# Optimization experiments

Hardware: AMD Instinct MI355X
Metric: run time of the kernel (lower is better)

## Reference

```python
import jax, jax.numpy as jnp
import numpy as np

N_HEADS, D_MODEL, DK, DV = 16, 1024, 64, 64
B, S = 4, 2048


def setup_inputs() -> dict:
    key = jax.random.key(0)
    ks = jax.random.split(key, 7)
    scale = 1.0 / np.sqrt(D_MODEL)
    return {
        "Q": jax.random.normal(ks[0], (B, S, D_MODEL), dtype=jnp.float32),
        "K": jax.random.normal(ks[1], (B, S, D_MODEL), dtype=jnp.float32),
        "V": jax.random.normal(ks[2], (B, S, D_MODEL), dtype=jnp.float32),
        # Linear weights stored as [in, out] so y = x @ W (equivalent to torch x @ W.T)
        "w_q": jax.random.normal(ks[3], (D_MODEL, N_HEADS * DK), dtype=jnp.float32) * scale,
        "w_k": jax.random.normal(ks[4], (D_MODEL, N_HEADS * DK), dtype=jnp.float32) * scale,
        "w_v": jax.random.normal(ks[5], (D_MODEL, N_HEADS * DV), dtype=jnp.float32) * scale,
        "w_o": jax.random.normal(ks[6], (N_HEADS * DV, D_MODEL), dtype=jnp.float32) * scale,
    }


def reference(Q, K, V, w_q, w_k, w_v, w_o):
    b, s, _ = Q.shape
    # projections -> [B, H, S, d]
    q = (Q @ w_q).reshape(b, s, N_HEADS, DK).transpose(0, 2, 1, 3)
    k = (K @ w_k).reshape(b, s, N_HEADS, DK).transpose(0, 2, 1, 3)
    v = (V @ w_v).reshape(b, s, N_HEADS, DV).transpose(0, 2, 1, 3)
    # scaled dot-product attention, full [B,H,S,S] scores (matches source)
    scores = jnp.einsum("bhqd,bhkd->bhqk", q, k) / jnp.sqrt(jnp.float32(DK))
    attn = jax.nn.softmax(scores, axis=-1)
    x = jnp.einsum("bhqk,bhkd->bhqd", attn, v)
    x = x.transpose(0, 2, 1, 3).reshape(b, s, N_HEADS * DV)
    return x @ w_o
```

## Files before the change

kernel.cpp:

```cpp
#include <hip/hip_runtime.h>
#include <stdint.h>

#define B_   4
#define S_   2048
#define H_   16
#define D_   64
#define DM_  1024
#define NTOK (B_ * S_)

typedef __attribute__((ext_vector_type(8))) short short8;
typedef __attribute__((ext_vector_type(4))) float floatx4;

__device__ inline unsigned short f2bf(float f) {
  unsigned int u = __float_as_uint(f);
  u += 0x7FFFu + ((u >> 16) & 1u);
  return (unsigned short)(u >> 16);
}

__device__ inline floatx4 mfma_bf16(short8 a, short8 b, floatx4 c) {
  return __builtin_amdgcn_mfma_f32_16x16x32_bf16(a, b, c, 0, 0, 0);
}

__device__ inline unsigned int pack_bf2(float lo, float hi) {
  return __builtin_amdgcn_perm(__float_as_uint(hi), __float_as_uint(lo), 0x07060302u);
}

__device__ inline void gload_lds16(const unsigned short* g, unsigned short* l) {
  __builtin_amdgcn_global_load_lds(
      (const __attribute__((address_space(1))) unsigned int*)g,
      (__attribute__((address_space(3))) unsigned int*)l, 16, 0, 0);
}

__global__ __launch_bounds__(256) void cast_bf16_kernel(const float* __restrict__ in,
                                                        unsigned short* __restrict__ out,
                                                        int n4) {
  int i = blockIdx.x * 256 + threadIdx.x;
  if (i < n4) {
    float4 v = ((const float4*)in)[i];
    ushort4 o;
    o.x = f2bf(v.x); o.y = f2bf(v.y); o.z = f2bf(v.z); o.w = f2bf(v.w);
    ((ushort4*)out)[i] = o;
  }
}

__global__ __launch_bounds__(256) void wt_kernel(const float* __restrict__ w0,
                                                 const float* __restrict__ w1,
                                                 const float* __restrict__ w2,
                                                 const float* __restrict__ w3,
                                                 unsigned short* __restrict__ o0,
                                                 unsigned short* __restrict__ o1,
                                                 unsigned short* __restrict__ o2,
                                                 unsigned short* __restrict__ o3) {
  __shared__ unsigned short T[64 * 68];
  const float* w = blockIdx.z == 0 ? w0 : blockIdx.z == 1 ? w1 : blockIdx.z == 2 ? w2 : w3;
  unsigned short* o = blockIdx.z == 0 ? o0 : blockIdx.z == 1 ? o1 : blockIdx.z == 2 ? o2 : o3;
  const int tid = threadIdx.x;
  const int R0 = blockIdx.y * 64;
  const int C0 = blockIdx.x * 64;
  for (int it = 0; it < 16; it++) {
    int lr = it * 4 + (tid >> 6), lc = tid & 63;
    T[lc * 68 + lr] = f2bf(w[(size_t)(R0 + lr) * 1024 + C0 + lc]);
  }
  __syncthreads();
  for (int it = 0; it < 2; it++) {
    int orow = it * 32 + (tid >> 3), oc = (tid & 7) * 8;
    union { ushort4 h[2]; short8 v8; } u;
    u.h[0] = *(const ushort4*)(T + orow * 68 + oc);
    u.h[1] = *(const ushort4*)(T + orow * 68 + oc + 4);
    *(short8*)(o + (size_t)(C0 + orow) * 1024 + R0 + oc) = u.v8;
  }
}

template <int MODE>
__global__ __launch_bounds__(256) void gemm_bt_kernel(const unsigned short* __restrict__ A,
                                                      const unsigned short* __restrict__ BT,
                                                      void* __restrict__ Cout,
                                                      float scale) {
  constexpr int K = 1024;
  __shared__ unsigned short As[128 * 32];
  __shared__ unsigned short Bs[128 * 32];

  const int tid  = threadIdx.x;
  const int wave = tid >> 6, lane = tid & 63;
  const int quad = lane >> 4, l16 = lane & 15;
  const int wm = wave >> 1, wn = wave & 1;
  const int m0 = blockIdx.y * 128, n0 = blockIdx.x * 128;

  floatx4 acc[4][4] = {};

  for (int k0 = 0; k0 < K; k0 += 32) {
    for (int p = 0; p < 2; p++) {
      int i = p * 256 + wave * 64 + lane;
      int row = i >> 2, c = i & 3;
      gload_lds16(A  + (size_t)(m0 + row) * K + k0 + c * 8,
                  As + (size_t)(p * 256 + wave * 64) * 8);
      gload_lds16(BT + (size_t)(n0 + row) * K + k0 + c * 8,
                  Bs + (size_t)(p * 256 + wave * 64) * 8);
    }
    __syncthreads();

    short8 af[4], bfr[4];
    for (int f = 0; f < 4; f++) {
      af[f]  = *(const short8*)(As + (wm * 64 + f * 16 + l16) * 32 + quad * 8);
      bfr[f] = *(const short8*)(Bs + (wn * 64 + f * 16 + l16) * 32 + quad * 8);
    }
    for (int fm = 0; fm < 4; fm++)
      for (int fn = 0; fn < 4; fn++)
        acc[fm][fn] = mfma_bf16(af[fm], bfr[fn], acc[fm][fn]);
    __syncthreads();
  }

  for (int fm = 0; fm < 4; fm++)
    for (int fn = 0; fn < 4; fn++)
      for (int r = 0; r < 4; r++) {
        int gm = m0 + wm * 64 + fm * 16 + quad * 4 + r;
        int gn = n0 + wn * 64 + fn * 16 + l16;
        float val = acc[fm][fn][r] * scale;
        if (MODE == 0) {
          int b = gm >> 11, s = gm & 2047;
          int h = gn >> 6,  d = gn & 63;
          ((unsigned short*)Cout)[((size_t)((b * H_ + h) * S_ + s) << 6) + d] = f2bf(val);
        } else if (MODE == 1) {
          ((float*)Cout)[((size_t)gm << 10) + gn] = val;
        } else {
          int b = gm >> 11, s = gm & 2047;
          int h = gn >> 6,  d = gn & 63;
          int p = ((s & 63) >> 4) + (s & 15) * 4;
          ((unsigned short*)Cout)[(((size_t)(b * H_ + h) * 64 + d) << 11) + (s & ~63) + p] = f2bf(val);
        }
      }
}

__global__ __launch_bounds__(256, 2) void attn_kernel(const unsigned short* __restrict__ q,
                                                      const unsigned short* __restrict__ k,
                                                      const unsigned short* __restrict__ vT,
                                                      unsigned short* __restrict__ X) {
  __shared__ unsigned short Ks[64 * 64];
  __shared__ unsigned short Vt[64 * 64];
  __shared__ unsigned short Ps[4][16 * 72];

  const int tid  = threadIdx.x;
  const int wave = tid >> 6, lane = tid & 63;
  const int quad = lane >> 4, l16 = lane & 15;
  const int bh = blockIdx.y;
  const int q0 = blockIdx.x * 256;

  const unsigned short* qh = q  + (size_t)bh * S_ * 64;
  const unsigned short* kh = k  + (size_t)bh * S_ * 64;
  const unsigned short* vh = vT + (size_t)bh * 64 * S_;

  short8 qf[4][2];
  for (int qt = 0; qt < 4; qt++) {
    int row = q0 + wave * 64 + qt * 16 + l16;
    for (int kk = 0; kk < 2; kk++)
      qf[qt][kk] = *(const short8*)(qh + (size_t)row * 64 + kk * 32 + quad * 8);
  }

  short8 onesb = {};
  if (l16 == 0)
    for (int e = 0; e < 8; e++) onesb[e] = (short)0x3F80;

  floatx4 O[4][4] = {};
  floatx4 lacc[4] = {};

  for (int j0 = 0; j0 < S_; j0 += 64) {
    __syncthreads();

    for (int p = 0; p < 2; p++) {
      int i = p * 256 + tid;
      int r = i >> 3;
      int gc = (i & 7) ^ (r & 7);
      gload_lds16(kh + (size_t)(j0 + r) * 64 + gc * 8,
                  Ks + (size_t)(p * 256 + wave * 64) * 8);
      gload_lds16(vh + (size_t)r * S_ + j0 + gc * 8,
                  Vt + (size_t)(p * 256 + wave * 64) * 8);
    }
    __syncthreads();

    short8 kf[4][2];
    for (int jf = 0; jf < 4; jf++)
      for (int kk = 0; kk < 2; kk++) {
        int sl = (kk * 4 + quad) ^ (l16 & 7);
        kf[jf][kk] = *(const short8*)(Ks + (jf * 16 + l16) * 64 + sl * 8);
      }
    short8 vf[4][2];
    for (int df = 0; df < 4; df++)
      for (int jk = 0; jk < 2; jk++) {
        int sl = (jk * 4 + quad) ^ (l16 & 7);
        vf[df][jk] = *(const short8*)(Vt + (df * 16 + l16) * 64 + sl * 8);
      }

    unsigned short* pw = Ps[wave];
    for (int qt = 0; qt < 4; qt++) {
      floatx4 s[4] = {};
      for (int jf = 0; jf < 4; jf++) {
        s[jf] = mfma_bf16(qf[qt][0], kf[jf][0], s[jf]);
        s[jf] = mfma_bf16(qf[qt][1], kf[jf][1], s[jf]);
      }
      for (int r = 0; r < 4; r++) {
        float e0 = exp2f(s[0][r]), e1 = exp2f(s[1][r]);
        float e2 = exp2f(s[2][r]), e3 = exp2f(s[3][r]);
        uint2 pk;
        pk.x = pack_bf2(e0, e1);
        pk.y = pack_bf2(e2, e3);
        *(uint2*)(pw + (quad * 4 + r) * 72 + l16 * 4) = pk;
      }
      short8 pa0 = *(const short8*)(pw + l16 * 72 + quad * 8);
      short8 pa1 = *(const short8*)(pw + l16 * 72 + 32 + quad * 8);
      lacc[qt] = mfma_bf16(pa0, onesb, lacc[qt]);
      lacc[qt] = mfma_bf16(pa1, onesb, lacc[qt]);
      for (int df = 0; df < 4; df++) {
        O[qt][df] = mfma_bf16(pa0, vf[df][0], O[qt][df]);
        O[qt][df] = mfma_bf16(pa1, vf[df][1], O[qt][df]);
      }
    }
  }

  const int b = bh >> 4, h = bh & 15;
  for (int qt = 0; qt < 4; qt++)
    for (int r = 0; r < 4; r++) {
      float lsum = __shfl(lacc[qt][r], (lane & 48));
      float inv = 1.0f / lsum;
      int row = q0 + wave * 64 + qt * 16 + quad * 4 + r;
      unsigned short* dst = X + ((size_t)(b * S_ + row) << 10) + h * 64;
      for (int df = 0; df < 4; df++)
        dst[df * 16 + l16] = f2bf(O[qt][df][r] * inv);
    }
}

extern "C" void kernel_launch(void* const* d_in, const int* in_sizes, int n_in,
                              void* d_out, int out_size, void* d_ws, size_t ws_size,
                              hipStream_t stream) {
  const float* Q  = (const float*)d_in[0];
  const float* K  = (const float*)d_in[1];
  const float* V  = (const float*)d_in[2];
  const float* wq = (const float*)d_in[3];
  const float* wk = (const float*)d_in[4];
  const float* wv = (const float*)d_in[5];
  const float* wo = (const float*)d_in[6];

  char* ws = (char*)d_ws;
  unsigned short* buf0 = (unsigned short*)ws;
  unsigned short* wqT  = (unsigned short*)(ws + (size_t)(16 << 20));
  unsigned short* wkT  = (unsigned short*)(ws + (size_t)(18 << 20));
  unsigned short* wvT  = (unsigned short*)(ws + (size_t)(20 << 20));
  unsigned short* woT  = (unsigned short*)(ws + (size_t)(22 << 20));
  unsigned short* qP   = (unsigned short*)(ws + (size_t)(24 << 20));
  unsigned short* kP   = (unsigned short*)(ws + (size_t)(40 << 20));
  unsigned short* vTg  = (unsigned short*)(ws + (size_t)(56 << 20));

  const int n4 = NTOK * DM_ / 4;
  const float SC = 0.18033688011112043f;

  wt_kernel<<<dim3(16, 16, 4), dim3(256), 0, stream>>>(wq, wk, wv, wo, wqT, wkT, wvT, woT);

  cast_bf16_kernel<<<dim3(8192), dim3(256), 0, stream>>>(Q, buf0, n4);
  gemm_bt_kernel<0><<<dim3(8, 64), dim3(256), 0, stream>>>(buf0, wqT, qP, SC);
  cast_bf16_kernel<<<dim3(8192), dim3(256), 0, stream>>>(K, buf0, n4);
  gemm_bt_kernel<0><<<dim3(8, 64), dim3(256), 0, stream>>>(buf0, wkT, kP, 1.0f);
  cast_bf16_kernel<<<dim3(8192), dim3(256), 0, stream>>>(V, buf0, n4);
  gemm_bt_kernel<2><<<dim3(8, 64), dim3(256), 0, stream>>>(buf0, wvT, vTg, 1.0f);

  attn_kernel<<<dim3(8, 64), dim3(256), 0, stream>>>(qP, kP, vTg, buf0);

  gemm_bt_kernel<1><<<dim3(8, 64), dim3(256), 0, stream>>>(buf0, woT, (float*)d_out, 1.0f);
}
```

Baseline: 376.9 us.

## Fuse fp32 cast into batched QKV GEMM and double-buffer LDS in all kernels

Removes the three separate fp32-to-bf16 cast kernels. The QKV projection now loads fp32 activations directly into swizzled LDS, converts them to bf16 in registers, and computes all three projections in a single launch. All GEMMs and the attention kernel switch to double-buffered LDS with async global-to-LDS prefetch of the next tile, which also drops one barrier per iteration. exp2f is replaced by the hardware exp2 builtin. The fp32 A tile doubles LDS traffic and footprint in the QKV GEMM, which could reduce occupancy.

```diff
diff --git a/kernel.cpp b/kernel.cpp
--- a/kernel.cpp
+++ b/kernel.cpp
@@ -1,4 +1,5 @@
 #include <hip/hip_runtime.h>
+#include <hip/hip_bf16.h>
 #include <stdint.h>
 
 #define B_   4
@@ -25,22 +26,16 @@
   return __builtin_amdgcn_perm(__float_as_uint(hi), __float_as_uint(lo), 0x07060302u);
 }
 
-__device__ inline void gload_lds16(const unsigned short* g, unsigned short* l) {
+__device__ inline unsigned int cvt_pk_bf16(float lo, float hi) {
+  __hip_bfloat162 h = __float22bfloat162_rn(make_float2(lo, hi));
+  return *(unsigned int*)&h;
+}
+
+template <typename T>
+__device__ inline void gload_lds16(const T* g, T* l) {
   __builtin_amdgcn_global_load_lds(
       (const __attribute__((address_space(1))) unsigned int*)g,
       (__attribute__((address_space(3))) unsigned int*)l, 16, 0, 0);
-}
-
-__global__ __launch_bounds__(256) void cast_bf16_kernel(const float* __restrict__ in,
-                                                        unsigned short* __restrict__ out,
-                                                        int n4) {
-  int i = blockIdx.x * 256 + threadIdx.x;
-  if (i < n4) {
-    float4 v = ((const float4*)in)[i];
-    ushort4 o;
-    o.x = f2bf(v.x); o.y = f2bf(v.y); o.z = f2bf(v.z); o.w = f2bf(v.w);
-    ((ushort4*)out)[i] = o;
-  }
 }
 
 __global__ __launch_bounds__(256) void wt_kernel(const float* __restrict__ w0,
@@ -71,14 +66,96 @@
   }
 }
 
-template <int MODE>
-__global__ __launch_bounds__(256) void gemm_bt_kernel(const unsigned short* __restrict__ A,
-                                                      const unsigned short* __restrict__ BT,
-                                                      void* __restrict__ Cout,
-                                                      float scale) {
+__global__ __launch_bounds__(256) void gemm_qkv_kernel(
+    const float* __restrict__ Qf, const float* __restrict__ Kf,
+    const float* __restrict__ Vf,
+    const unsigned short* __restrict__ wqT, const unsigned short* __restrict__ wkT,
+    const unsigned short* __restrict__ wvT,
+    unsigned short* __restrict__ qP, unsigned short* __restrict__ kP,
+    unsigned short* __restrict__ vTg, float SC) {
   constexpr int K = 1024;
-  __shared__ unsigned short As[128 * 32];
-  __shared__ unsigned short Bs[128 * 32];
+  __shared__ float          As[2][128 * 32];
+  __shared__ unsigned short Bs[2][128 * 32];
+
+  const int tid  = threadIdx.x;
+  const int wave = tid >> 6, lane = tid & 63;
+  const int quad = lane >> 4, l16 = lane & 15;
+  const int wm = wave >> 1, wn = wave & 1;
+  const int z  = blockIdx.x >> 3;
+  const int n0 = (blockIdx.x & 7) * 128;
+  const int m0 = blockIdx.y * 128;
+
+  const float* A = z == 0 ? Qf : z == 1 ? Kf : Vf;
+  const unsigned short* BT = z == 0 ? wqT : z == 1 ? wkT : wvT;
+
+  floatx4 acc[4][4] = {};
+
+  auto stage = [&](int buf, int k0) {
+    for (int p = 0; p < 4; p++) {
+      int i = p * 256 + wave * 64 + lane;
+      int r = i >> 3, gc = (i & 7) ^ (r & 7);
+      gload_lds16(A + (size_t)(m0 + r) * K + k0 + gc * 4,
+                  &As[buf][(p * 256 + wave * 64) * 4]);
+    }
+    for (int p = 0; p < 2; p++) {
+      int i = p * 256 + wave * 64 + lane;
+      int r = i >> 2, c = i & 3;
+      gload_lds16(BT + (size_t)(n0 + r) * K + k0 + c * 8,
+                  &Bs[buf][(p * 256 + wave * 64) * 8]);
+    }
+  };
+
+  stage(0, 0);
+  for (int kt = 0; kt < K / 32; kt++) {
+    __syncthreads();
+    if (kt + 1 < K / 32) stage((kt + 1) & 1, (kt + 1) * 32);
+    const int cur = kt & 1;
+
+    short8 af[4], bfr[4];
+    for (int f = 0; f < 4; f++) {
+      int row = wm * 64 + f * 16 + l16;
+      int s0 = row * 8 + ((quad * 2)     ^ (row & 7));
+      int s1 = row * 8 + ((quad * 2 + 1) ^ (row & 7));
+      float4 a0 = *(const float4*)&As[cur][s0 * 4];
+      float4 a1 = *(const float4*)&As[cur][s1 * 4];
+      union { unsigned int u[4]; short8 v; } t;
+      t.u[0] = cvt_pk_bf16(a0.x, a0.y);
+      t.u[1] = cvt_pk_bf16(a0.z, a0.w);
+      t.u[2] = cvt_pk_bf16(a1.x, a1.y);
+      t.u[3] = cvt_pk_bf16(a1.z, a1.w);
+      af[f]  = t.v;
+      bfr[f] = *(const short8*)&Bs[cur][(wn * 64 + f * 16 + l16) * 32 + quad * 8];
+    }
+    for (int fm = 0; fm < 4; fm++)
+      for (int fn = 0; fn < 4; fn++)
+        acc[fm][fn] = mfma_bf16(af[fm], bfr[fn], acc[fm][fn]);
+  }
+
+  for (int fm = 0; fm < 4; fm++)
+    for (int fn = 0; fn < 4; fn++)
+      for (int r = 0; r < 4; r++) {
+        int gm = m0 + wm * 64 + fm * 16 + quad * 4 + r;
+        int gn = n0 + wn * 64 + fn * 16 + l16;
+        int b = gm >> 11, s = gm & 2047;
+        int h = gn >> 6,  d = gn & 63;
+        float val = acc[fm][fn][r];
+        if (z == 0) {
+          qP[((size_t)((b * H_ + h) * S_ + s) << 6) + d] = f2bf(val * SC);
+        } else if (z == 1) {
+          kP[((size_t)((b * H_ + h) * S_ + s) << 6) + d] = f2bf(val);
+        } else {
+          int p = ((s & 63) >> 4) + (s & 15) * 4;
+          vTg[(((size_t)(b * H_ + h) * 64 + d) << 11) + (s & ~63) + p] = f2bf(val);
+        }
+      }
+}
+
+__global__ __launch_bounds__(256) void gemm_out_kernel(const unsigned short* __restrict__ A,
+                                                       const unsigned short* __restrict__ BT,
+                                                       float* __restrict__ C) {
+  constexpr int K = 1024;
+  __shared__ unsigned short As[2][128 * 32];
+  __shared__ unsigned short Bs[2][128 * 32];
 
   const int tid  = threadIdx.x;
   const int wave = tid >> 6, lane = tid & 63;
@@ -88,26 +165,31 @@
 
   floatx4 acc[4][4] = {};
 
-  for (int k0 = 0; k0 < K; k0 += 32) {
+  auto stage = [&](int buf, int k0) {
     for (int p = 0; p < 2; p++) {
       int i = p * 256 + wave * 64 + lane;
-      int row = i >> 2, c = i & 3;
-      gload_lds16(A  + (size_t)(m0 + row) * K + k0 + c * 8,
-                  As + (size_t)(p * 256 + wave * 64) * 8);
-      gload_lds16(BT + (size_t)(n0 + row) * K + k0 + c * 8,
-                  Bs + (size_t)(p * 256 + wave * 64) * 8);
-    }
+      int r = i >> 2, c = i & 3;
+      gload_lds16(A  + (size_t)(m0 + r) * K + k0 + c * 8,
+                  &As[buf][(p * 256 + wave * 64) * 8]);
+      gload_lds16(BT + (size_t)(n0 + r) * K + k0 + c * 8,
+                  &Bs[buf][(p * 256 + wave * 64) * 8]);
+    }
+  };
+
+  stage(0, 0);
+  for (int kt = 0; kt < K / 32; kt++) {
     __syncthreads();
+    if (kt + 1 < K / 32) stage((kt + 1) & 1, (kt + 1) * 32);
+    const int cur = kt & 1;
 
     short8 af[4], bfr[4];
     for (int f = 0; f < 4; f++) {
-      af[f]  = *(const short8*)(As + (wm * 64 + f * 16 + l16) * 32 + quad * 8);
-      bfr[f] = *(const short8*)(Bs + (wn * 64 + f * 16 + l16) * 32 + quad * 8);
+      af[f]  = *(const short8*)&As[cur][(wm * 64 + f * 16 + l16) * 32 + quad * 8];
+      bfr[f] = *(const short8*)&Bs[cur][(wn * 64 + f * 16 + l16) * 32 + quad * 8];
     }
     for (int fm = 0; fm < 4; fm++)
       for (int fn = 0; fn < 4; fn++)
         acc[fm][fn] = mfma_bf16(af[fm], bfr[fn], acc[fm][fn]);
-    __syncthreads();
   }
 
   for (int fm = 0; fm < 4; fm++)
@@ -115,19 +197,7 @@
       for (int r = 0; r < 4; r++) {
         int gm = m0 + wm * 64 + fm * 16 + quad * 4 + r;
         int gn = n0 + wn * 64 + fn * 16 + l16;
-        float val = acc[fm][fn][r] * scale;
-        if (MODE == 0) {
-          int b = gm >> 11, s = gm & 2047;
-          int h = gn >> 6,  d = gn & 63;
-          ((unsigned short*)Cout)[((size_t)((b * H_ + h) * S_ + s) << 6) + d] = f2bf(val);
-        } else if (MODE == 1) {
-          ((float*)Cout)[((size_t)gm << 10) + gn] = val;
-        } else {
-          int b = gm >> 11, s = gm & 2047;
-          int h = gn >> 6,  d = gn & 63;
-          int p = ((s & 63) >> 4) + (s & 15) * 4;
-          ((unsigned short*)Cout)[(((size_t)(b * H_ + h) * 64 + d) << 11) + (s & ~63) + p] = f2bf(val);
-        }
+        C[((size_t)gm << 10) + gn] = acc[fm][fn][r];
       }
 }
 
@@ -135,8 +205,8 @@
                                                       const unsigned short* __restrict__ k,
                                                       const unsigned short* __restrict__ vT,
                                                       unsigned short* __restrict__ X) {
-  __shared__ unsigned short Ks[64 * 64];
-  __shared__ unsigned short Vt[64 * 64];
+  __shared__ unsigned short Ks[2][64 * 64];
+  __shared__ unsigned short Vt[2][64 * 64];
   __shared__ unsigned short Ps[4][16 * 72];
 
   const int tid  = threadIdx.x;
@@ -163,31 +233,35 @@
   floatx4 O[4][4] = {};
   floatx4 lacc[4] = {};
 
-  for (int j0 = 0; j0 < S_; j0 += 64) {
-    __syncthreads();
-
+  auto stage = [&](int buf, int j0) {
     for (int p = 0; p < 2; p++) {
       int i = p * 256 + tid;
       int r = i >> 3;
       int gc = (i & 7) ^ (r & 7);
       gload_lds16(kh + (size_t)(j0 + r) * 64 + gc * 8,
-                  Ks + (size_t)(p * 256 + wave * 64) * 8);
+                  &Ks[buf][(size_t)(p * 256 + wave * 64) * 8]);
       gload_lds16(vh + (size_t)r * S_ + j0 + gc * 8,
-                  Vt + (size_t)(p * 256 + wave * 64) * 8);
-    }
+                  &Vt[buf][(size_t)(p * 256 + wave * 64) * 8]);
+    }
+  };
+
+  stage(0, 0);
+  for (int jt = 0; jt < S_ / 64; jt++) {
     __syncthreads();
+    if (jt + 1 < S_ / 64) stage((jt + 1) & 1, (jt + 1) * 64);
+    const int cur = jt & 1;
 
     short8 kf[4][2];
     for (int jf = 0; jf < 4; jf++)
       for (int kk = 0; kk < 2; kk++) {
         int sl = (kk * 4 + quad) ^ (l16 & 7);
-        kf[jf][kk] = *(const short8*)(Ks + (jf * 16 + l16) * 64 + sl * 8);
+        kf[jf][kk] = *(const short8*)&Ks[cur][(jf * 16 + l16) * 64 + sl * 8];
       }
     short8 vf[4][2];
     for (int df = 0; df < 4; df++)
       for (int jk = 0; jk < 2; jk++) {
         int sl = (jk * 4 + quad) ^ (l16 & 7);
-        vf[df][jk] = *(const short8*)(Vt + (df * 16 + l16) * 64 + sl * 8);
+        vf[df][jk] = *(const short8*)&Vt[cur][(df * 16 + l16) * 64 + sl * 8];
       }
 
     unsigned short* pw = Ps[wave];
@@ -198,8 +272,10 @@
         s[jf] = mfma_bf16(qf[qt][1], kf[jf][1], s[jf]);
       }
       for (int r = 0; r < 4; r++) {
-        float e0 = exp2f(s[0][r]), e1 = exp2f(s[1][r]);
-        float e2 = exp2f(s[2][r]), e3 = exp2f(s[3][r]);
+        float e0 = __builtin_amdgcn_exp2f(s[0][r]);
+        float e1 = __builtin_amdgcn_exp2f(s[1][r]);
+        float e2 = __builtin_amdgcn_exp2f(s[2][r]);
+        float e3 = __builtin_amdgcn_exp2f(s[3][r]);
         uint2 pk;
         pk.x = pack_bf2(e0, e1);
         pk.y = pack_bf2(e2, e3);
@@ -249,19 +325,14 @@
   unsigned short* kP   = (unsigned short*)(ws + (size_t)(40 << 20));
   unsigned short* vTg  = (unsigned short*)(ws + (size_t)(56 << 20));
 
-  const int n4 = NTOK * DM_ / 4;
   const float SC = 0.18033688011112043f;
 
   wt_kernel<<<dim3(16, 16, 4), dim3(256), 0, stream>>>(wq, wk, wv, wo, wqT, wkT, wvT, woT);
 
-  cast_bf16_kernel<<<dim3(8192), dim3(256), 0, stream>>>(Q, buf0, n4);
-  gemm_bt_kernel<0><<<dim3(8, 64), dim3(256), 0, stream>>>(buf0, wqT, qP, SC);
-  cast_bf16_kernel<<<dim3(8192), dim3(256), 0, stream>>>(K, buf0, n4);
-  gemm_bt_kernel<0><<<dim3(8, 64), dim3(256), 0, stream>>>(buf0, wkT, kP, 1.0f);
-  cast_bf16_kernel<<<dim3(8192), dim3(256), 0, stream>>>(V, buf0, n4);
-  gemm_bt_kernel<2><<<dim3(8, 64), dim3(256), 0, stream>>>(buf0, wvT, vTg, 1.0f);
+  gemm_qkv_kernel<<<dim3(24, 64), dim3(256), 0, stream>>>(Q, K, V, wqT, wkT, wvT,
+                                                          qP, kP, vTg, SC);
 
   attn_kernel<<<dim3(8, 64), dim3(256), 0, stream>>>(qP, kP, vTg, buf0);
 
-  gemm_bt_kernel<1><<<dim3(8, 64), dim3(256), 0, stream>>>(buf0, woT, (float*)d_out, 1.0f);
-}
+  gemm_out_kernel<<<dim3(8, 64), dim3(256), 0, stream>>>(buf0, woT, (float*)d_out);
+}
```

Result: slower. 1.263 ms (+235.0%).
